# Optimization experiments

Measured on AMD Instinct MI355X. Metric: run time of the kernel, lower is better.

## Reference

```python
import jax, jax.numpy as jnp
import numpy as np

D = 1024
H = 16
HD = D // H
EPS = 1e-5

def _layernorm(x, g, b):
    xf = x.astype(jnp.float32)
    mu = jnp.mean(xf, axis=-1, keepdims=True)
    var = jnp.mean(jnp.square(xf - mu), axis=-1, keepdims=True)
    return ((xf - mu) * jax.lax.rsqrt(var + EPS) * g + b).astype(x.dtype)

def setup_inputs() -> dict:
    key = jax.random.key(0)
    ks = jax.random.split(key, 12)
    B, S = 4, 1024
    s_in = 1.0 / np.sqrt(D)
    inp = {
        "x": jax.random.normal(ks[0], (B, S, D), dtype=jnp.float32),
        "in_proj_w": jax.random.normal(ks[1], (3 * D, D), dtype=jnp.float32) * s_in,
        "in_proj_b": jnp.zeros((3 * D,), dtype=jnp.float32),
        "out_w": jax.random.normal(ks[2], (D, D), dtype=jnp.float32) * s_in,
        "out_b": jnp.zeros((D,), dtype=jnp.float32),
        "ln1_g": jnp.ones((D,), dtype=jnp.float32),
        "ln1_b": jnp.zeros((D,), dtype=jnp.float32),
        "fc_w": jax.random.normal(ks[3], (4 * D, D), dtype=jnp.float32) * s_in,
        "fc_b": jnp.zeros((4 * D,), dtype=jnp.float32),
        "proj_w": jax.random.normal(ks[4], (D, 4 * D), dtype=jnp.float32) * (1.0 / np.sqrt(4 * D)),
        "proj_b": jnp.zeros((D,), dtype=jnp.float32),
        "ln2_g": jnp.ones((D,), dtype=jnp.float32),
        "ln2_b": jnp.zeros((D,), dtype=jnp.float32),
    }
    return inp

def reference(x, in_proj_w, in_proj_b, out_w, out_b, ln1_g, ln1_b,
              fc_w, fc_b, proj_w, proj_b, ln2_g, ln2_b):
    B, S, _ = x.shape
    scaling = float(HD) ** -0.5
    # --- attention sublayer ---
    h = _layernorm(x, ln1_g, ln1_b)
    qkv = h @ in_proj_w.T + in_proj_b              # [B,S,3D]
    q, k, v = jnp.split(qkv, 3, axis=-1)
    q = (q * scaling).reshape(B, S, H, HD).transpose(0, 2, 1, 3)  # [B,H,S,hd]
    k = k.reshape(B, S, H, HD).transpose(0, 2, 1, 3)
    v = v.reshape(B, S, H, HD).transpose(0, 2, 1, 3)
    attn = jax.nn.softmax(jnp.einsum('bhqd,bhkd->bhqk', q, k), axis=-1)
    o = jnp.einsum('bhqk,bhkd->bhqd', attn, v).transpose(0, 2, 1, 3).reshape(B, S, D)
    x = x + o @ out_w.T + out_b
    # --- MLP sublayer (QuickGELU) ---
    h = _layernorm(x, ln2_g, ln2_b)
    u = h @ fc_w.T + fc_b                          # [B,S,4D]
    u = u * jax.nn.sigmoid(1.702 * u)
    x = x + u @ proj_w.T + proj_b
    return x
```

## Files before the change

### kernel.cpp

```cpp
#include <hip/hip_runtime.h>
#include <math.h>

#define D_MODEL 1024
#define SEQ     1024
#define BATCH   4
#define NTOK    (BATCH * SEQ)

typedef __bf16 bf16;
using bfrag  = __attribute__((ext_vector_type(8))) __bf16;
using ffrag  = __attribute__((ext_vector_type(4))) float;
using f32x16 = __attribute__((ext_vector_type(16))) float;

__device__ __forceinline__ ffrag mfma16(bfrag a, bfrag b, ffrag c) {
  return __builtin_amdgcn_mfma_f32_16x16x32_bf16(a, b, c, 0, 0, 0);
}
__device__ __forceinline__ f32x16 mfma32(bfrag a, bfrag b, f32x16 c) {
  return __builtin_amdgcn_mfma_f32_32x32x16_bf16(a, b, c, 0, 0, 0);
}
__device__ __forceinline__ unsigned cvt_pk(float lo, float hi) {
  unsigned r;
  asm("v_cvt_pk_bf16_f32 %0, %1, %2" : "=v"(r) : "v"(lo), "v"(hi));
  return r;
}

__device__ __forceinline__ void gload_lds16(const void* g, void* l) {
  __builtin_amdgcn_global_load_lds(
      (const __attribute__((address_space(1))) void*)g,
      (__attribute__((address_space(3))) void*)l, 16, 0, 0);
}

__device__ __forceinline__ int xcd_remap(int flat, int nwg) {
  return (flat & 7) * (nwg >> 3) + (flat >> 3);
}

__global__ void convert_all(const float* __restrict__ s0, bf16* __restrict__ d0, int n0,
                            const float* __restrict__ s1, bf16* __restrict__ d1, int n1,
                            const float* __restrict__ s2, bf16* __restrict__ d2, int n2,
                            const float* __restrict__ s3, bf16* __restrict__ d3, int n3,
                            float scale, int limit0) {
  const float* src; bf16* dst; int n; int limit = 0;
  switch (blockIdx.y) {
    case 0: src = s0; dst = d0; n = n0; limit = limit0; break;
    case 1: src = s1; dst = d1; n = n1; break;
    case 2: src = s2; dst = d2; n = n2; break;
    default: src = s3; dst = d3; n = n3; break;
  }
  int i = blockIdx.x * blockDim.x + threadIdx.x;
  const int stride = gridDim.x * blockDim.x;
  for (; i < n; i += stride) {
    float4 v = ((const float4*)src)[i];
    float sc = (i < limit) ? scale : 1.0f;
    bf16* d = dst + (size_t)i * 4;
    d[0] = (bf16)(v.x * sc); d[1] = (bf16)(v.y * sc);
    d[2] = (bf16)(v.z * sc); d[3] = (bf16)(v.w * sc);
  }
}

__global__ void scale_bias(const float* __restrict__ src, float* __restrict__ dst,
                           int n, int limit, float scale) {
  int i = blockIdx.x * blockDim.x + threadIdx.x;
  if (i < n) dst[i] = src[i] * (i < limit ? scale : 1.0f);
}

__global__ __launch_bounds__(256) void ln_row(const float* __restrict__ x,
                                              const float* __restrict__ gamma,
                                              const float* __restrict__ beta,
                                              bf16* __restrict__ out) {
  const int row = blockIdx.x, tid = threadIdx.x;
  const float4 v = ((const float4*)(x + (size_t)row * D_MODEL))[tid];
  float s  = v.x + v.y + v.z + v.w;
  float ss = v.x * v.x + v.y * v.y + v.z * v.z + v.w * v.w;
#pragma unroll
  for (int off = 32; off >= 1; off >>= 1) {
    s  += __shfl_xor(s, off);
    ss += __shfl_xor(ss, off);
  }
  __shared__ float rs[4], rss[4];
  const int w = tid >> 6;
  if ((tid & 63) == 0) { rs[w] = s; rss[w] = ss; }
  __syncthreads();
  s  = rs[0] + rs[1] + rs[2] + rs[3];
  ss = rss[0] + rss[1] + rss[2] + rss[3];
  const float mu   = s * (1.0f / D_MODEL);
  const float var  = ss * (1.0f / D_MODEL) - mu * mu;
  const float rstd = rsqrtf(var + 1e-5f);
  const float4 gv = ((const float4*)gamma)[tid];
  const float4 bv = ((const float4*)beta)[tid];
  bf16* o = out + (size_t)row * D_MODEL + tid * 4;
  o[0] = (bf16)((v.x - mu) * rstd * gv.x + bv.x);
  o[1] = (bf16)((v.y - mu) * rstd * gv.y + bv.y);
  o[2] = (bf16)((v.z - mu) * rstd * gv.z + bv.z);
  o[3] = (bf16)((v.w - mu) * rstd * gv.w + bv.w);
}

template <int EPI>
__global__ __launch_bounds__(256, 4) void gemm_bt(
    const bf16* __restrict__ A, const bf16* __restrict__ B,
    const float* __restrict__ bias, const float* __restrict__ resid,
    float* __restrict__ outF, bf16* __restrict__ outB,
    int M, int N, int K) {
  __shared__ bf16 As[2][128 * 32];
  __shared__ bf16 Bs[2][128 * 32];
  const int tid = threadIdx.x;
  const int lane = tid & 63, w = tid >> 6;
  const int wm = w >> 1, wn = w & 1;
  const int ql = lane & 15, lg = lane >> 4;
  const int nwg = gridDim.x * gridDim.y;
  const int flat = xcd_remap(blockIdx.y * gridDim.x + blockIdx.x, nwg);
  const int m0 = (flat % gridDim.x) * 128, n0 = (flat / gridDim.x) * 128;

  ffrag acc[4][4];
#pragma unroll
  for (int i = 0; i < 4; i++)
#pragma unroll
    for (int j = 0; j < 4; j++) acc[i][j] = ffrag{0.f, 0.f, 0.f, 0.f};

  const int r0 = tid >> 2;
  const int jsw = (tid & 3) ^ ((r0 >> 1) & 3);
  const bf16* a0 = A + (size_t)(m0 + r0) * K + jsw * 8;
  const bf16* a1 = A + (size_t)(m0 + 64 + r0) * K + jsw * 8;
  const bf16* b0 = B + (size_t)(n0 + r0) * K + jsw * 8;
  const bf16* b1 = B + (size_t)(n0 + 64 + r0) * K + jsw * 8;
  const int lo = w * 512;

  auto STAGE = [&](int bs, int kk) {
    gload_lds16(a0 + kk, &As[bs][lo]);
    gload_lds16(a1 + kk, &As[bs][2048 + lo]);
    gload_lds16(b0 + kk, &Bs[bs][lo]);
    gload_lds16(b1 + kk, &Bs[bs][2048 + lo]);
  };

  STAGE(0, 0);
  __syncthreads();

  int cur = 0;
  for (int k0 = 0; k0 < K; k0 += 32) {
    if (k0 + 32 < K) STAGE(cur ^ 1, k0 + 32);
    bfrag af[4], bfr[4];
#pragma unroll
    for (int i = 0; i < 4; i++) {
      const int row = wm * 64 + i * 16 + ql;
      af[i] = *(const bfrag*)&As[cur][row * 32 + ((lg ^ ((row >> 1) & 3)) * 8)];
    }
#pragma unroll
    for (int j = 0; j < 4; j++) {
      const int row = wn * 64 + j * 16 + ql;
      bfr[j] = *(const bfrag*)&Bs[cur][row * 32 + ((lg ^ ((row >> 1) & 3)) * 8)];
    }
#pragma unroll
    for (int i = 0; i < 4; i++)
#pragma unroll
      for (int j = 0; j < 4; j++)
        acc[i][j] = mfma16(af[i], bfr[j], acc[i][j]);
    __syncthreads();
    cur ^= 1;
  }

#pragma unroll
  for (int i = 0; i < 4; i++) {
    const int row = m0 + wm * 64 + i * 16 + lg * 4;
#pragma unroll
    for (int j = 0; j < 4; j++) {
      const int col = n0 + wn * 64 + j * 16 + ql;
      const float bv = bias[col];
#pragma unroll
      for (int r = 0; r < 4; r++) {
        float v = acc[i][j][r] + bv;
        const size_t idx = (size_t)(row + r) * N + col;
        if (EPI == 0) {
          outB[idx] = (bf16)v;
        } else if (EPI == 1) {
          outF[idx] = v + resid[idx];
        } else {
          outB[idx] = (bf16)(v / (1.0f + __expf(-1.702f * v)));
        }
      }
    }
  }
}

template <int EPI>
__global__ __launch_bounds__(256, 4) void gemm_bt64(
    const bf16* __restrict__ A, const bf16* __restrict__ B,
    const float* __restrict__ bias, const float* __restrict__ resid,
    float* __restrict__ outF, bf16* __restrict__ outB,
    int M, int N, int K) {
  __shared__ bf16 As[2][64 * 64];
  __shared__ bf16 Bs[2][64 * 64];
  const int tid = threadIdx.x;
  const int lane = tid & 63, w = tid >> 6;
  const int wm = w >> 1, wn = w & 1;
  const int ql = lane & 15, lg = lane >> 4;
  const int bid = blockIdx.x;
  const int k8 = bid & 7, j8 = bid >> 3;
  const int m0 = (k8 * 8 + (j8 & 7)) * 64;
  const int n0 = (j8 >> 3) * 64;

  ffrag acc[2][2];
#pragma unroll
  for (int i = 0; i < 2; i++)
#pragma unroll
    for (int j = 0; j < 2; j++) acc[i][j] = ffrag{0.f, 0.f, 0.f, 0.f};

  const int r0 = tid >> 3;
  const int jsw = ((tid & 7) ^ (r0 & 7)) * 8;
  const bf16* a0 = A + (size_t)(m0 + r0) * K + jsw;
  const bf16* a1 = A + (size_t)(m0 + 32 + r0) * K + jsw;
  const bf16* b0 = B + (size_t)(n0 + r0) * K + jsw;
  const bf16* b1 = B + (size_t)(n0 + 32 + r0) * K + jsw;
  const int lo = tid * 8;

  auto STAGE = [&](int bs, int kk) {
    gload_lds16(a0 + kk, &As[bs][lo]);
    gload_lds16(a1 + kk, &As[bs][2048 + lo]);
    gload_lds16(b0 + kk, &Bs[bs][lo]);
    gload_lds16(b1 + kk, &Bs[bs][2048 + lo]);
  };

  STAGE(0, 0);
  __syncthreads();

  int cur = 0;
  for (int k0 = 0; k0 < K; k0 += 64) {
    if (k0 + 64 < K) STAGE(cur ^ 1, k0 + 64);
    bfrag af[2][2], bfr[2][2];
#pragma unroll
    for (int i = 0; i < 2; i++) {
      const int row = wm * 32 + i * 16 + ql;
      const int r7 = row & 7;
#pragma unroll
      for (int kc = 0; kc < 2; kc++)
        af[i][kc] = *(const bfrag*)&As[cur][row * 64 + (((lg + 4 * kc) ^ r7) * 8)];
    }
#pragma unroll
    for (int j = 0; j < 2; j++) {
      const int row = wn * 32 + j * 16 + ql;
      const int r7 = row & 7;
#pragma unroll
      for (int kc = 0; kc < 2; kc++)
        bfr[j][kc] = *(const bfrag*)&Bs[cur][row * 64 + (((lg + 4 * kc) ^ r7) * 8)];
    }
#pragma unroll
    for (int kc = 0; kc < 2; kc++)
#pragma unroll
      for (int i = 0; i < 2; i++)
#pragma unroll
        for (int j = 0; j < 2; j++)
          acc[i][j] = mfma16(af[i][kc], bfr[j][kc], acc[i][j]);
    __syncthreads();
    cur ^= 1;
  }

#pragma unroll
  for (int i = 0; i < 2; i++) {
    const int row = m0 + wm * 32 + i * 16 + lg * 4;
#pragma unroll
    for (int j = 0; j < 2; j++) {
      const int col = n0 + wn * 32 + j * 16 + ql;
      const float bv = bias[col];
#pragma unroll
      for (int r = 0; r < 4; r++) {
        float v = acc[i][j][r] + bv;
        const size_t idx = (size_t)(row + r) * N + col;
        if (EPI == 0) {
          outB[idx] = (bf16)v;
        } else if (EPI == 1) {
          outF[idx] = v + resid[idx];
        } else {
          outB[idx] = (bf16)(v / (1.0f + __expf(-1.702f * v)));
        }
      }
    }
  }
}

__global__ __launch_bounds__(256) void transpose_v(const bf16* __restrict__ qkv,
                                                   bf16* __restrict__ vt) {
  __shared__ bf16 T[64 * 66];
  const int tid = threadIdx.x;
  const int bh = blockIdx.y, b = bh >> 4, h = bh & 15;
  const int s0 = blockIdx.x * 64;
  const bf16* src = qkv + (size_t)b * SEQ * 3072 + 2048 + h * 64;

  const int sl = tid >> 3, c = tid & 7;
#pragma unroll
  for (int p = 0; p < 2; p++) {
    const int s = sl + p * 32;
    const bfrag v = *(const bfrag*)(src + (size_t)(s0 + s) * 3072 + c * 8);
#pragma unroll
    for (int e = 0; e < 8; e++) T[s * 66 + c * 8 + e] = v[e];
  }
  __syncthreads();
  bf16* dst = vt + (size_t)bh * 64 * 1024;
#pragma unroll
  for (int p = 0; p < 2; p++) {
    const int d = sl + p * 32;
    bfrag o;
#pragma unroll
    for (int e = 0; e < 8; e++) o[e] = T[(c * 8 + e) * 66 + d];
    *(bfrag*)(dst + (size_t)d * 1024 + s0 + c * 8) = o;
  }
}

__global__ __launch_bounds__(256, 2) void flash_attn(const bf16* __restrict__ qkv,
                                                     const bf16* __restrict__ vt,
                                                     bf16* __restrict__ o) {
  __shared__ bf16 Kl[2][128 * 64];
  __shared__ bf16 Vl[2][64 * 128];
  __shared__ float RB[4][32];
  const int tid = threadIdx.x, lane = tid & 63, wid = tid >> 6;
  const int l31 = lane & 31, hi = lane >> 5;
  const int flat = xcd_remap(blockIdx.y * 8 + blockIdx.x, 512);
  const int qblk = flat & 7, bh = flat >> 3, b = bh >> 4, h = bh & 15;
  const int qb0 = qblk * 128 + wid * 32;
  const size_t headq = (size_t)b * SEQ * 3072 + (size_t)h * 64;

  const bf16* qp = qkv + headq + (size_t)(qb0 + l31) * 3072 + hi * 8;
  bfrag qb[4];
#pragma unroll
  for (int t = 0; t < 4; t++) qb[t] = *(const bfrag*)(qp + t * 16);

  float mrun = -1e30f, lrun = 0.0f;
  f32x16 oacc[2];
#pragma unroll
  for (int r = 0; r < 16; r++) { oacc[0][r] = 0.f; oacc[1][r] = 0.f; }

  const int ksrc = ((tid & 7) ^ ((tid >> 3) & 7) ^ wid) * 8;
  const bf16* kp = qkv + headq + 1024 + (size_t)(tid >> 3) * 3072 + ksrc;
  const bf16* vhead = vt + (size_t)bh * 64 * 1024;
  const int xlane = (l31 & 7) ^ (l31 >> 3);

  auto STAGE = [&](int bs, int kt) {
#pragma unroll
    for (int pp = 0; pp < 4; pp++)
      gload_lds16(kp + (size_t)(kt + pp * 32) * 3072, &Kl[bs][pp * 2048 + tid * 8]);
#pragma unroll
    for (int pp = 0; pp < 4; pp++) {
      const int vr = pp * 16 + (tid >> 4);
      const int gc = (tid & 15) ^ ((tid >> 4) & 7) ^ ((pp * 2 + (tid >> 7)) & 3);
      gload_lds16(vhead + (size_t)vr * 1024 + kt + gc * 8, &Vl[bs][(pp * 256 + tid) * 8]);
    }
  };

  STAGE(0, 0);
  __syncthreads();

  int cur = 0;
  for (int kt = 0; kt < SEQ; kt += 128) {
    if (kt + 128 < SEQ) STAGE(cur ^ 1, kt + 128);

    f32x16 sacc[4];
#pragma unroll
    for (int s = 0; s < 4; s++)
#pragma unroll
      for (int r = 0; r < 16; r++) sacc[s][r] = 0.f;
    __builtin_amdgcn_s_setprio(1);
#pragma unroll
    for (int s = 0; s < 4; s++) {
      const int krow = s * 32 + l31;
#pragma unroll
      for (int t = 0; t < 4; t++) {
        const int ch = (t * 2) ^ hi ^ xlane;
        const bfrag kf = *(const bfrag*)&Kl[cur][krow * 64 + ch * 8];
        sacc[s] = mfma32(kf, qb[t], sacc[s]);
      }
    }
    __builtin_amdgcn_s_setprio(0);

    float lm = sacc[0][0];
#pragma unroll
    for (int s = 0; s < 4; s++)
#pragma unroll
      for (int r = 0; r < 16; r++) lm = fmaxf(lm, sacc[s][r]);

    if (!__all(lm - mrun <= 8.0f)) {
      const float mx = fmaxf(lm, __shfl_xor(lm, 32));
      const float mnew = fmaxf(mrun, mx);
      const float corr = exp2f(mrun - mnew);
      mrun = mnew;
      lrun *= corr;
      if (!hi) RB[wid][l31] = corr;
#pragma unroll
      for (int r = 0; r < 16; r++) {
        const float c = RB[wid][(r & 3) + 8 * (r >> 2) + 4 * hi];
        oacc[0][r] *= c;
        oacc[1][r] *= c;
      }
    }

#pragma unroll
    for (int s = 0; s < 4; s++) {
      float p[16];
#pragma unroll
      for (int r = 0; r < 16; r++) p[r] = exp2f(sacc[s][r] - mrun);
#pragma unroll
      for (int r = 0; r < 16; r++) lrun += p[r];
      const unsigned A = cvt_pk(p[0], p[1]),  B = cvt_pk(p[2], p[3]);
      const unsigned C = cvt_pk(p[4], p[5]),  D = cvt_pk(p[6], p[7]);
      const unsigned E = cvt_pk(p[8], p[9]),  F = cvt_pk(p[10], p[11]);
      const unsigned G = cvt_pk(p[12], p[13]), H = cvt_pk(p[14], p[15]);
      const unsigned x1 = __shfl_xor(hi ? A : C, 32);
      const unsigned x2 = __shfl_xor(hi ? B : D, 32);
      const unsigned x3 = __shfl_xor(hi ? E : G, 32);
      const unsigned x4 = __shfl_xor(hi ? F : H, 32);
      unsigned w0[4] = { hi ? x1 : A, hi ? x2 : B, hi ? C : x1, hi ? D : x2 };
      unsigned w1[4] = { hi ? x3 : E, hi ? x4 : F, hi ? G : x3, hi ? H : x4 };
      const bfrag pa0 = *(const bfrag*)w0;
      const bfrag pa1 = *(const bfrag*)w1;
      __builtin_amdgcn_s_setprio(1);
#pragma unroll
      for (int db = 0; db < 2; db++) {
        const int vrow = db * 32 + l31;
        const bfrag vf0 = *(const bfrag*)&Vl[cur][vrow * 128 + ((((2 * s) * 2) ^ hi ^ xlane) & 15) * 8];
        oacc[db] = mfma32(pa0, vf0, oacc[db]);
        const bfrag vf1 = *(const bfrag*)&Vl[cur][vrow * 128 + ((((2 * s + 1) * 2) ^ hi ^ xlane) & 15) * 8];
        oacc[db] = mfma32(pa1, vf1, oacc[db]);
      }
      __builtin_amdgcn_s_setprio(0);
    }
    __syncthreads();
    cur ^= 1;
  }

  const float lsum = lrun + __shfl_xor(lrun, 32);
  if (!hi) RB[wid][l31] = 1.0f / lsum;
#pragma unroll
  for (int r = 0; r < 16; r++) {
    const int qml = (r & 3) + 8 * (r >> 2) + 4 * hi;
    const float rv = RB[wid][qml];
    const size_t orow = (size_t)b * SEQ + qb0 + qml;
    o[orow * 1024 + h * 64 + l31]      = (bf16)(oacc[0][r] * rv);
    o[orow * 1024 + h * 64 + 32 + l31] = (bf16)(oacc[1][r] * rv);
  }
}

extern "C" void kernel_launch(void* const* d_in, const int* in_sizes, int n_in,
                              void* d_out, int out_size, void* d_ws, size_t ws_size,
                              hipStream_t stream) {
  (void)in_sizes; (void)n_in; (void)out_size; (void)ws_size;
  const float* x      = (const float*)d_in[0];
  const float* in_w   = (const float*)d_in[1];
  const float* in_b   = (const float*)d_in[2];
  const float* out_w  = (const float*)d_in[3];
  const float* out_b  = (const float*)d_in[4];
  const float* ln1_g  = (const float*)d_in[5];
  const float* ln1_b  = (const float*)d_in[6];
  const float* fc_w   = (const float*)d_in[7];
  const float* fc_b   = (const float*)d_in[8];
  const float* proj_w = (const float*)d_in[9];
  const float* proj_b = (const float*)d_in[10];
  const float* ln2_g  = (const float*)d_in[11];
  const float* ln2_b  = (const float*)d_in[12];
  float* out = (float*)d_out;

  char* p = (char*)d_ws;
  auto alloc = [&](size_t bytes) { char* r = p; p += (bytes + 255) & ~255ull; return r; };
  bf16* w_qkv  = (bf16*)alloc((size_t)3072 * 1024 * 2);
  bf16* w_out  = (bf16*)alloc((size_t)1024 * 1024 * 2);
  bf16* w_fc   = (bf16*)alloc((size_t)4096 * 1024 * 2);
  bf16* w_proj = (bf16*)alloc((size_t)1024 * 4096 * 2);
  float* b_qkv = (float*)alloc((size_t)3072 * 4);
  bf16* hbuf   = (bf16*)alloc((size_t)NTOK * 1024 * 2);
  float* x2    = (float*)alloc((size_t)NTOK * 1024 * 4);
  bf16* qkv    = (bf16*)alloc((size_t)NTOK * 3072 * 2);
  bf16* aout   = (bf16*)alloc((size_t)NTOK * 1024 * 2);
  bf16* ubuf   = qkv;
  bf16* vtb    = (bf16*)x2;

  const float scaling = 0.125f * 1.44269504089f;
  convert_all<<<dim3(1024, 4), 256, 0, stream>>>(
      in_w, w_qkv, 3072 * 1024 / 4,
      out_w, w_out, 1024 * 1024 / 4,
      fc_w, w_fc, 4096 * 1024 / 4,
      proj_w, w_proj, 4096 * 1024 / 4,
      scaling, 1024 * 1024 / 4);
  scale_bias<<<12, 256, 0, stream>>>(in_b, b_qkv, 3072, 1024, scaling);

  ln_row<<<NTOK, 256, 0, stream>>>(x, ln1_g, ln1_b, hbuf);
  gemm_bt<0><<<dim3(32, 24), 256, 0, stream>>>(hbuf, w_qkv, b_qkv, nullptr,
                                               nullptr, qkv, NTOK, 3072, 1024);
  transpose_v<<<dim3(16, 64), 256, 0, stream>>>(qkv, vtb);
  flash_attn<<<dim3(8, 64), 256, 0, stream>>>(qkv, vtb, aout);
  gemm_bt64<1><<<1024, 256, 0, stream>>>(aout, w_out, out_b, x,
                                         x2, nullptr, NTOK, 1024, 1024);
  ln_row<<<NTOK, 256, 0, stream>>>(x2, ln2_g, ln2_b, hbuf);
  gemm_bt<2><<<dim3(32, 32), 256, 0, stream>>>(hbuf, w_fc, fc_b, nullptr,
                                               nullptr, ubuf, NTOK, 4096, 1024);
  gemm_bt64<1><<<1024, 256, 0, stream>>>(ubuf, w_proj, proj_b, x2,
                                         out, nullptr, NTOK, 1024, 4096);
}
```

Baseline: 217.1 us.

## Replace 128x128 GEMM with 256x256 tiled, quadrant-pipelined 512-thread GEMM

The QKV and FC projection GEMMs move from a 128x128x32 tile kernel with 256 threads to a 256x256x64 tile kernel with 512 threads and 128KB of dynamic LDS. Each k-step is split into four quadrants so that LDS fragment loads, MFMA bursts and global-to-LDS prefetch of the next tile interleave, using raw barriers, explicit waitcnt and setprio. The larger tile raises arithmetic intensity and cuts global traffic per FLOP. In exchange the grid is small (192 and 256 blocks), the 128KB LDS footprint limits occupancy to one block per CU, and the hand-placed barriers risk fragile ordering.

New measurement: 218.6 us. No clear change (+0.7%).

```diff
diff --git a/kernel.cpp b/kernel.cpp
--- a/kernel.cpp
+++ b/kernel.cpp
@@ -27,6 +27,12 @@
   __builtin_amdgcn_global_load_lds(
       (const __attribute__((address_space(1))) void*)g,
       (__attribute__((address_space(3))) void*)l, 16, 0, 0);
+}
+
+__device__ __forceinline__ void barrier_raw() {
+  asm volatile("" ::: "memory");
+  __builtin_amdgcn_s_barrier();
+  asm volatile("" ::: "memory");
 }
 
 __device__ __forceinline__ int xcd_remap(int flat, int nwg) {
@@ -94,86 +100,135 @@
 }
 
 template <int EPI>
-__global__ __launch_bounds__(256, 4) void gemm_bt(
+__global__ __launch_bounds__(512, 2) void gemm256(
     const bf16* __restrict__ A, const bf16* __restrict__ B,
-    const float* __restrict__ bias, const float* __restrict__ resid,
-    float* __restrict__ outF, bf16* __restrict__ outB,
+    const float* __restrict__ bias, bf16* __restrict__ outB,
     int M, int N, int K) {
-  __shared__ bf16 As[2][128 * 32];
-  __shared__ bf16 Bs[2][128 * 32];
+  extern __shared__ bf16 sm[];
   const int tid = threadIdx.x;
-  const int lane = tid & 63, w = tid >> 6;
-  const int wm = w >> 1, wn = w & 1;
+  const int lane = tid & 63, wid = tid >> 6;
+  const int wm = wid >> 2, wn = wid & 3;
   const int ql = lane & 15, lg = lane >> 4;
-  const int nwg = gridDim.x * gridDim.y;
-  const int flat = xcd_remap(blockIdx.y * gridDim.x + blockIdx.x, nwg);
-  const int m0 = (flat % gridDim.x) * 128, n0 = (flat / gridDim.x) * 128;
-
-  ffrag acc[4][4];
-#pragma unroll
-  for (int i = 0; i < 4; i++)
-#pragma unroll
-    for (int j = 0; j < 4; j++) acc[i][j] = ffrag{0.f, 0.f, 0.f, 0.f};
-
-  const int r0 = tid >> 2;
-  const int jsw = (tid & 3) ^ ((r0 >> 1) & 3);
-  const bf16* a0 = A + (size_t)(m0 + r0) * K + jsw * 8;
-  const bf16* a1 = A + (size_t)(m0 + 64 + r0) * K + jsw * 8;
-  const bf16* b0 = B + (size_t)(n0 + r0) * K + jsw * 8;
-  const bf16* b1 = B + (size_t)(n0 + 64 + r0) * K + jsw * 8;
-  const int lo = w * 512;
-
-  auto STAGE = [&](int bs, int kk) {
-    gload_lds16(a0 + kk, &As[bs][lo]);
-    gload_lds16(a1 + kk, &As[bs][2048 + lo]);
-    gload_lds16(b0 + kk, &Bs[bs][lo]);
-    gload_lds16(b1 + kk, &Bs[bs][2048 + lo]);
+  const int gx = M >> 8;
+  const int flat = xcd_remap(blockIdx.x, gridDim.x);
+  const int m0 = (flat % gx) << 8, n0 = (flat / gx) << 8;
+
+  auto aslot = [&](int buf, int half) { return sm + ((buf * 2 + half) << 13); };
+  auto bslot = [&](int buf, int half) { return sm + 32768 + ((buf * 2 + half) << 13); };
+
+  ffrag acc[8][4];
+#pragma unroll
+  for (int a = 0; a < 8; a++)
+#pragma unroll
+    for (int b = 0; b < 4; b++) acc[a][b] = ffrag{0.f, 0.f, 0.f, 0.f};
+
+  const int r0 = tid >> 3;
+  const int jsw = ((tid & 7) ^ (r0 & 7)) * 8;
+  const bf16* ag = A + (size_t)(m0 + r0) * K + jsw;
+  const bf16* bg = B + (size_t)(n0 + r0) * K + jsw;
+
+  auto STAGE_A = [&](int bs, int half, int kk) {
+    bf16* d = aslot(bs, half);
+    gload_lds16(ag + (size_t)(half * 128) * K + kk, d + tid * 8);
+    gload_lds16(ag + (size_t)(half * 128 + 64) * K + kk, d + 4096 + tid * 8);
   };
-
-  STAGE(0, 0);
-  __syncthreads();
-
-  int cur = 0;
-  for (int k0 = 0; k0 < K; k0 += 32) {
-    if (k0 + 32 < K) STAGE(cur ^ 1, k0 + 32);
-    bfrag af[4], bfr[4];
+  auto STAGE_B = [&](int bs, int half, int kk) {
+    bf16* d = bslot(bs, half);
+    gload_lds16(bg + (size_t)(half * 128) * K + kk, d + tid * 8);
+    gload_lds16(bg + (size_t)(half * 128 + 64) * K + kk, d + 4096 + tid * 8);
+  };
+
+  bfrag af[4][2], bfr[2][2];
+  auto LOADQ = [&](int q, int buf) {
+    const int qm = q >> 1, qn = q & 1;
+    const bf16* as = aslot(buf, wm);
+    const bf16* bs = bslot(buf, wn >> 1);
 #pragma unroll
     for (int i = 0; i < 4; i++) {
-      const int row = wm * 64 + i * 16 + ql;
-      af[i] = *(const bfrag*)&As[cur][row * 32 + ((lg ^ ((row >> 1) & 3)) * 8)];
-    }
-#pragma unroll
-    for (int j = 0; j < 4; j++) {
-      const int row = wn * 64 + j * 16 + ql;
-      bfr[j] = *(const bfrag*)&Bs[cur][row * 32 + ((lg ^ ((row >> 1) & 3)) * 8)];
-    }
-#pragma unroll
-    for (int i = 0; i < 4; i++)
-#pragma unroll
-      for (int j = 0; j < 4; j++)
-        acc[i][j] = mfma16(af[i], bfr[j], acc[i][j]);
-    __syncthreads();
-    cur ^= 1;
-  }
-
-#pragma unroll
-  for (int i = 0; i < 4; i++) {
-    const int row = m0 + wm * 64 + i * 16 + lg * 4;
-#pragma unroll
-    for (int j = 0; j < 4; j++) {
-      const int col = n0 + wn * 64 + j * 16 + ql;
+      const int rih = qm * 64 + i * 16 + ql;
+#pragma unroll
+      for (int kc = 0; kc < 2; kc++)
+        af[i][kc] = *(const bfrag*)&as[rih * 64 + (((kc * 4 + lg) ^ (rih & 7)) * 8)];
+    }
+#pragma unroll
+    for (int j = 0; j < 2; j++) {
+      const int cih = (wn & 1) * 64 + qn * 32 + j * 16 + ql;
+#pragma unroll
+      for (int kc = 0; kc < 2; kc++)
+        bfr[j][kc] = *(const bfrag*)&bs[cih * 64 + (((kc * 4 + lg) ^ (cih & 7)) * 8)];
+    }
+  };
+  auto MFMAQ = [&](int q) {
+    const int qm = q >> 1, qn = q & 1;
+    __builtin_amdgcn_s_setprio(1);
+#pragma unroll
+    for (int kc = 0; kc < 2; kc++)
+#pragma unroll
+      for (int i = 0; i < 4; i++)
+#pragma unroll
+        for (int j = 0; j < 2; j++)
+          acc[qm * 4 + i][qn * 2 + j] =
+              mfma16(af[i][kc], bfr[j][kc], acc[qm * 4 + i][qn * 2 + j]);
+    __builtin_amdgcn_s_setprio(0);
+  };
+
+  STAGE_A(0, 0, 0); STAGE_A(0, 1, 0); STAGE_B(0, 0, 0); STAGE_B(0, 1, 0);
+
+  const int NT = K >> 6;
+  for (int t = 0; t < NT; ++t) {
+    const int buf = t & 1, nxt = buf ^ 1;
+    const int kn = (t + 1) << 6;
+    const bool pf = (t + 1 < NT);
+    if (pf) {
+      STAGE_A(nxt, 0, kn);
+      asm volatile("s_waitcnt vmcnt(2)" ::: "memory");
+    } else {
+      asm volatile("s_waitcnt vmcnt(0)" ::: "memory");
+    }
+    barrier_raw();
+    __builtin_amdgcn_sched_barrier(0);
+    LOADQ(0, buf);
+    asm volatile("s_waitcnt lgkmcnt(0)" ::: "memory");
+    __builtin_amdgcn_sched_barrier(0);
+    MFMAQ(0);
+    barrier_raw();
+    LOADQ(1, buf);
+    if (pf) STAGE_A(nxt, 1, kn);
+    barrier_raw();
+    asm volatile("s_waitcnt lgkmcnt(0)" ::: "memory");
+    __builtin_amdgcn_sched_barrier(0);
+    MFMAQ(1);
+    barrier_raw();
+    LOADQ(2, buf);
+    if (pf) STAGE_B(nxt, 0, kn);
+    barrier_raw();
+    asm volatile("s_waitcnt lgkmcnt(0)" ::: "memory");
+    __builtin_amdgcn_sched_barrier(0);
+    MFMAQ(2);
+    barrier_raw();
+    LOADQ(3, buf);
+    if (pf) STAGE_B(nxt, 1, kn);
+    barrier_raw();
+    asm volatile("s_waitcnt lgkmcnt(0)" ::: "memory");
+    __builtin_amdgcn_sched_barrier(0);
+    MFMAQ(3);
+    barrier_raw();
+  }
+  asm volatile("" ::: "memory");
+
+#pragma unroll
+  for (int a = 0; a < 8; a++) {
+    const int row = m0 + wm * 128 + (a >> 2) * 64 + (a & 3) * 16 + lg * 4;
+#pragma unroll
+    for (int b = 0; b < 4; b++) {
+      const int col = n0 + wn * 64 + (b >> 1) * 32 + (b & 1) * 16 + ql;
       const float bv = bias[col];
 #pragma unroll
       for (int r = 0; r < 4; r++) {
-        float v = acc[i][j][r] + bv;
+        float v = acc[a][b][r] + bv;
         const size_t idx = (size_t)(row + r) * N + col;
-        if (EPI == 0) {
-          outB[idx] = (bf16)v;
-        } else if (EPI == 1) {
-          outF[idx] = v + resid[idx];
-        } else {
-          outB[idx] = (bf16)(v / (1.0f + __expf(-1.702f * v)));
-        }
+        if (EPI == 0) outB[idx] = (bf16)v;
+        else          outB[idx] = (bf16)(v / (1.0f + __expf(-1.702f * v)));
       }
     }
   }
@@ -477,15 +532,15 @@
   scale_bias<<<12, 256, 0, stream>>>(in_b, b_qkv, 3072, 1024, scaling);
 
   ln_row<<<NTOK, 256, 0, stream>>>(x, ln1_g, ln1_b, hbuf);
-  gemm_bt<0><<<dim3(32, 24), 256, 0, stream>>>(hbuf, w_qkv, b_qkv, nullptr,
-                                               nullptr, qkv, NTOK, 3072, 1024);
+  gemm256<0><<<16 * 12, 512, 131072, stream>>>(hbuf, w_qkv, b_qkv, qkv,
+                                               NTOK, 3072, 1024);
   transpose_v<<<dim3(16, 64), 256, 0, stream>>>(qkv, vtb);
   flash_attn<<<dim3(8, 64), 256, 0, stream>>>(qkv, vtb, aout);
   gemm_bt64<1><<<1024, 256, 0, stream>>>(aout, w_out, out_b, x,
                                          x2, nullptr, NTOK, 1024, 1024);
   ln_row<<<NTOK, 256, 0, stream>>>(x2, ln2_g, ln2_b, hbuf);
-  gemm_bt<2><<<dim3(32, 32), 256, 0, stream>>>(hbuf, w_fc, fc_b, nullptr,
-                                               nullptr, ubuf, NTOK, 4096, 1024);
+  gemm256<2><<<16 * 16, 512, 131072, stream>>>(hbuf, w_fc, fc_b, ubuf,
+                                               NTOK, 4096, 1024);
   gemm_bt64<1><<<1024, 256, 0, stream>>>(ubuf, w_proj, proj_b, x2,
                                          out, nullptr, NTOK, 1024, 4096);
 }
```
